# Kernel optimization log

Hardware: AMD Instinct MI355X
Metric: run time of the kernel (lower is better)

## Reference

```python
import jax, jax.numpy as jnp
import numpy as np

MASK_NEG = 1e30


def setup_inputs() -> dict:
    key = jax.random.key(0)
    k_q, k_k, k_m, k_w1, k_w2, k_v = jax.random.split(key, 6)
    B, S, D, A = 32, 2048, 1024, 1024  # batch, seq, feature dim, attn dim
    # Xavier-uniform-like scale for weights
    lim = float(np.sqrt(6.0 / (D + A)))
    query = jax.random.normal(k_q, (B, D), dtype=jnp.float32)
    keys = jax.random.normal(k_k, (B, S, D), dtype=jnp.float32)
    mask = jax.random.randint(k_m, (B, S), 0, 2) > 0  # True = keep
    W1 = jax.random.uniform(k_w1, (A, D), jnp.float32, -lim, lim)
    W2 = jax.random.uniform(k_w2, (A, D), jnp.float32, -lim, lim)
    v = jax.random.uniform(k_v, (A,), jnp.float32, -lim, lim)
    return {"query": query, "keys": keys, "mask": mask, "W1": W1, "W2": W2, "v": v}


def reference(query, keys, mask, W1, W2, v):
    w1_query = jnp.einsum('bd,ad->ba', query, W1)          # (B, A)
    w2_keys = jnp.einsum('bsd,ad->bsa', keys, W2)          # (B, S, A)
    combined = jnp.tanh(w1_query[:, None, :] + w2_keys)    # (B, S, A)
    scores = jnp.einsum('bsa,a->bs', combined, v)          # (B, S)
    # masked softmax: subtract huge constant at masked-out positions
    scores = scores - (~mask).astype(scores.dtype) * MASK_NEG
    return jax.nn.softmax(scores, axis=-1)
```

## Files before the change

kernel.cpp:

```cpp
#include <hip/hip_runtime.h>
#include <hip/hip_bf16.h>
#include <stdint.h>

#define NB 32
#define NS 2048
#define ND 1024
#define NA 1024
#define MASK_NEG 1e30f

#define BM 256
#define BN 256
#define BK 64
#define NTILES 64

typedef __attribute__((ext_vector_type(4))) float f32x4;
typedef __attribute__((ext_vector_type(8))) __bf16 bf16x8;

__device__ __forceinline__ void glds16(const void* g, void* l) {
  __builtin_amdgcn_global_load_lds(
      (const __attribute__((address_space(1))) uint32_t*)g,
      (__attribute__((address_space(3))) uint32_t*)(uintptr_t)l, 16, 0, 0);
}

__global__ __launch_bounds__(256) void cvt_bf16(const float* __restrict__ in,
                                                __bf16* __restrict__ out, int n8) {
  long i = blockIdx.x * 256 + threadIdx.x;
  const long stride = (long)gridDim.x * 256;
  for (; i < n8; i += stride) {
    f32x4 a = ((const f32x4*)in)[2 * i];
    f32x4 b = ((const f32x4*)in)[2 * i + 1];
    bf16x8 o;
#pragma unroll
    for (int j = 0; j < 4; ++j) { o[j] = (__bf16)a[j]; o[4 + j] = (__bf16)b[j]; }
    ((bf16x8*)out)[i] = o;
  }
}

__global__ __launch_bounds__(256) void w1q_kernel(const float* __restrict__ q,
                                                  const float* __restrict__ W1,
                                                  float* __restrict__ w1q) {
  const int b = blockIdx.x;
  const int a0 = blockIdx.y * 64;
  const int t = threadIdx.x;
  const int al = t >> 2;
  const int part = t & 3;
  const float* wrow = W1 + (size_t)(a0 + al) * ND + part * 256;
  const float* qrow = q + (size_t)b * ND + part * 256;
  float sum = 0.f;
#pragma unroll 8
  for (int i = 0; i < 256; i += 4) {
    float4 w = *reinterpret_cast<const float4*>(wrow + i);
    float4 x = *reinterpret_cast<const float4*>(qrow + i);
    sum += w.x * x.x + w.y * x.y + w.z * x.z + w.w * x.w;
  }
  __shared__ float red[256];
  red[t] = sum;
  __syncthreads();
  if (t < 64) {
    w1q[(size_t)b * NA + a0 + t] = red[t * 4] + red[t * 4 + 1] + red[t * 4 + 2] + red[t * 4 + 3];
  }
}

__global__ __launch_bounds__(512, 1) void score_gemm8(
    const __bf16* __restrict__ keysb, const __bf16* __restrict__ W2b,
    const float* __restrict__ w1q, const float* __restrict__ vvec,
    float* __restrict__ scores) {
  __shared__ __bf16 ldsA[4][128 * BK];
  __shared__ __bf16 ldsB[4][128 * BK];
  __shared__ float sm_w1q[NA];
  __shared__ float sm_v[NA];
  __shared__ float sm_part[4][BM];

  const int t = threadIdx.x;
  const int bs0 = blockIdx.x * BM;
  const int b = bs0 >> 11;
  const int lane = t & 63;
  const int wid = t >> 6;
  const int wr = wid >> 2;
  const int wc = wid & 3;
  const int lrow = lane & 15;
  const int ko = lane >> 4;

  for (int i = t; i < NA; i += 512) {
    sm_w1q[i] = w1q[(size_t)b * NA + i];
    sm_v[i] = vvec[i];
  }
  for (int i = t; i < 4 * BM; i += 512) ((float*)sm_part)[i] = 0.f;

  const int srow = lane >> 3;
  const int scol = (lane & 7) ^ srow;
  const size_t aoffT = (size_t)(bs0 + wid * 16 + srow) * ND + scol * 8;
  const size_t boffT = (size_t)(wid * 16 + srow) * ND + scol * 8;

  const int sl0 = ko ^ (lrow & 7);
  const int sl1 = (4 + ko) ^ (lrow & 7);

#define STAGE_A(T, H)                                                           \
  do {                                                                          \
    if ((T) < NTILES) {                                                         \
      char* d_ = (char*)ldsA + (((((T)&1) << 1) + (H)) << 14) + wid * 2048;     \
      const size_t g_ = aoffT + (size_t)((H)*128) * ND + (size_t)(((T)&15) * BK); \
      glds16(keysb + g_, d_);                                                   \
      glds16(keysb + g_ + (size_t)8 * ND, d_ + 1024);                           \
    }                                                                           \
  } while (0)

#define STAGE_B(T, H)                                                           \
  do {                                                                          \
    if ((T) < NTILES) {                                                         \
      char* d_ = (char*)ldsB + (((((T)&1) << 1) + (H)) << 14) + wid * 2048;     \
      const size_t g_ = boffT + (size_t)(((T) >> 4) * 256 + (H)*128) * ND +     \
                        (size_t)(((T)&15) * BK);                                \
      glds16(W2b + g_, d_);                                                     \
      glds16(W2b + g_ + (size_t)8 * ND, d_ + 1024);                             \
    }                                                                           \
  } while (0)

#define SB __builtin_amdgcn_sched_barrier(0)
#define P1 __builtin_amdgcn_s_setprio(1)
#define P0 __builtin_amdgcn_s_setprio(0)
#define BAR __builtin_amdgcn_s_barrier()

#define PHASE(TL, M_, N_, STAGE_STMT, WM)                                       \
  do {                                                                          \
    if ((N_) == 0) {                                                            \
      const char* Ab_ = (const char*)ldsA + (((((TL)&1) << 1) | wr) << 14);     \
      _Pragma("unroll") for (int mi = 0; mi < 4; ++mi) {                        \
        const int ra_ = (((M_)*4 + mi) * 16 + lrow) * 128;                      \
        af[mi][0] = *reinterpret_cast<const bf16x8*>(Ab_ + ra_ + sl0 * 16);     \
        af[mi][1] = *reinterpret_cast<const bf16x8*>(Ab_ + ra_ + sl1 * 16);     \
      }                                                                         \
    }                                                                           \
    {                                                                           \
      const char* Bb_ = (const char*)ldsB + (((((TL)&1) << 1) | (wc >> 1)) << 14); \
      _Pragma("unroll") for (int nq = 0; nq < 2; ++nq) {                        \
        const int rb_ = (((wc & 1) * 4 + (N_)*2 + nq) * 16 + lrow) * 128;       \
        bfr[nq][0] = *reinterpret_cast<const bf16x8*>(Bb_ + rb_ + sl0 * 16);    \
        bfr[nq][1] = *reinterpret_cast<const bf16x8*>(Bb_ + rb_ + sl1 * 16);    \
      }                                                                         \
    }                                                                           \
    STAGE_STMT;                                                                 \
    BAR;                                                                        \
    asm volatile("s_waitcnt lgkmcnt(0)");                                       \
    SB;                                                                         \
    P1;                                                                         \
    _Pragma("unroll") for (int mi = 0; mi < 4; ++mi)                            \
        _Pragma("unroll") for (int nq = 0; nq < 2; ++nq) {                      \
      acc[(M_)*4 + mi][(N_)*2 + nq] = __builtin_amdgcn_mfma_f32_16x16x32_bf16(  \
          af[mi][0], bfr[nq][0], acc[(M_)*4 + mi][(N_)*2 + nq], 0, 0, 0);       \
      acc[(M_)*4 + mi][(N_)*2 + nq] = __builtin_amdgcn_mfma_f32_16x16x32_bf16(  \
          af[mi][1], bfr[nq][1], acc[(M_)*4 + mi][(N_)*2 + nq], 0, 0, 0);       \
    }                                                                           \
    P0;                                                                         \
    if (WM) {                                                                   \
      if (it != 31) { asm volatile("s_waitcnt vmcnt(2)"); }                     \
      else { asm volatile("s_waitcnt vmcnt(0)"); }                              \
      SB;                                                                       \
    }                                                                           \
    BAR;                                                                        \
  } while (0)

  f32x4 acc[8][4];
#pragma unroll
  for (int mi = 0; mi < 8; ++mi)
#pragma unroll
    for (int ni = 0; ni < 4; ++ni) acc[mi][ni] = f32x4{0.f, 0.f, 0.f, 0.f};

  bf16x8 af[4][2], bfr[2][2];

  STAGE_A(0, 0);
  STAGE_A(0, 1);
  STAGE_B(0, 0);
  STAGE_B(0, 1);
  STAGE_A(1, 0);
  __syncthreads();

  for (int it = 0; it < 32; ++it) {
    const int t0 = 2 * it, t1 = 2 * it + 1;
    PHASE(t0, 0, 0, STAGE_A(t1, 1), 0);
    PHASE(t0, 0, 1, STAGE_B(t1, 0), 0);
    PHASE(t0, 1, 0, STAGE_B(t1, 1), 0);
    PHASE(t0, 1, 1, STAGE_A(t0 + 2, 0), 1);
    PHASE(t1, 0, 0, STAGE_A(t0 + 2, 1), 0);
    PHASE(t1, 0, 1, STAGE_B(t0 + 2, 0), 0);
    PHASE(t1, 1, 0, STAGE_B(t0 + 2, 1), 0);
    PHASE(t1, 1, 1, STAGE_A(t1 + 2, 0), 1);

    if ((it & 7) == 7) {
      const int a0 = (it >> 3) * BN;
      float w1v[4], vv[4];
#pragma unroll
      for (int ni = 0; ni < 4; ++ni) {
        const int a = a0 + wc * 64 + ni * 16 + lrow;
        w1v[ni] = sm_w1q[a];
        vv[ni] = sm_v[a];
      }
#pragma unroll
      for (int mi = 0; mi < 8; ++mi)
#pragma unroll
        for (int r = 0; r < 4; ++r) {
          float p = 0.f;
#pragma unroll
          for (int ni = 0; ni < 4; ++ni) {
            const float x = acc[mi][ni][r] + w1v[ni];
            const float e = __expf(2.f * x);
            p += (1.f - 2.f * __builtin_amdgcn_rcpf(e + 1.f)) * vv[ni];
          }
          p += __shfl_xor(p, 1);
          p += __shfl_xor(p, 2);
          p += __shfl_xor(p, 4);
          p += __shfl_xor(p, 8);
          if (lrow == 0) sm_part[wc][wr * 128 + mi * 16 + ko * 4 + r] += p;
        }
#pragma unroll
      for (int mi = 0; mi < 8; ++mi)
#pragma unroll
        for (int ni = 0; ni < 4; ++ni) acc[mi][ni] = f32x4{0.f, 0.f, 0.f, 0.f};
    }
  }

  __syncthreads();
  if (t < BM)
    scores[bs0 + t] = sm_part[0][t] + sm_part[1][t] + sm_part[2][t] + sm_part[3][t];

#undef STAGE_A
#undef STAGE_B
#undef PHASE
#undef SB
#undef P1
#undef P0
#undef BAR
}

__global__ __launch_bounds__(256) void softmax_kernel(const float* __restrict__ scores,
                                                      const int* __restrict__ mask,
                                                      float* __restrict__ out) {
  const int b = blockIdx.x;
  const int t = threadIdx.x;
  float sc[8];
  float mx = -3.4e38f;
#pragma unroll
  for (int j = 0; j < 8; ++j) {
    int i = t + j * 256;
    float s = scores[b * NS + i];
    if (mask[b * NS + i] == 0) s -= MASK_NEG;
    sc[j] = s;
    mx = fmaxf(mx, s);
  }
#pragma unroll
  for (int off = 1; off < 64; off <<= 1) mx = fmaxf(mx, __shfl_xor(mx, off));
  __shared__ float redm[4];
  __shared__ float reds[4];
  if ((t & 63) == 0) redm[t >> 6] = mx;
  __syncthreads();
  mx = fmaxf(fmaxf(redm[0], redm[1]), fmaxf(redm[2], redm[3]));
  float e[8];
  float sum = 0.f;
#pragma unroll
  for (int j = 0; j < 8; ++j) {
    e[j] = __expf(sc[j] - mx);
    sum += e[j];
  }
#pragma unroll
  for (int off = 1; off < 64; off <<= 1) sum += __shfl_xor(sum, off);
  if ((t & 63) == 0) reds[t >> 6] = sum;
  __syncthreads();
  sum = reds[0] + reds[1] + reds[2] + reds[3];
  float inv = 1.f / sum;
#pragma unroll
  for (int j = 0; j < 8; ++j) out[b * NS + t + j * 256] = e[j] * inv;
}

extern "C" void kernel_launch(void* const* d_in, const int* in_sizes, int n_in,
                              void* d_out, int out_size, void* d_ws, size_t ws_size,
                              hipStream_t stream) {
  const float* q = (const float*)d_in[0];
  const float* keysf = (const float*)d_in[1];
  const int* mask = (const int*)d_in[2];
  const float* W1 = (const float*)d_in[3];
  const float* W2f = (const float*)d_in[4];
  const float* v = (const float*)d_in[5];
  float* out = (float*)d_out;

  float* scores = (float*)d_ws;
  float* w1q = scores + NB * NS;
  __bf16* W2b = (__bf16*)(w1q + NB * NA);
  __bf16* keysb = (__bf16*)((char*)W2b + (size_t)NA * ND * 2);

  cvt_bf16<<<512, 256, 0, stream>>>(W2f, W2b, NA * ND / 8);
  cvt_bf16<<<2048, 256, 0, stream>>>(keysf, keysb, (int)((size_t)NB * NS * ND / 8));
  w1q_kernel<<<dim3(NB, NA / 64), 256, 0, stream>>>(q, W1, w1q);
  score_gemm8<<<NB * NS / BM, 512, 0, stream>>>(keysb, W2b, w1q, v, scores);
  softmax_kernel<<<NB, 256, 0, stream>>>(scores, mask, out);
}
```

Measured before the change: 253.2 us.

## Fuse fp32-to-bf16 keys conversion into score GEMM loads

```diff
diff --git a/kernel.cpp b/kernel.cpp
--- a/kernel.cpp
+++ b/kernel.cpp
@@ -20,6 +20,11 @@
   __builtin_amdgcn_global_load_lds(
       (const __attribute__((address_space(1))) uint32_t*)g,
       (__attribute__((address_space(3))) uint32_t*)(uintptr_t)l, 16, 0, 0);
+}
+
+__global__ void zero_f32(float* __restrict__ p, int n) {
+  int i = blockIdx.x * 256 + threadIdx.x;
+  if (i < n) p[i] = 0.f;
 }
 
 __global__ __launch_bounds__(256) void cvt_bf16(const float* __restrict__ in,
@@ -61,15 +66,12 @@
   }
 }
 
-__global__ __launch_bounds__(512, 1) void score_gemm8(
-    const __bf16* __restrict__ keysb, const __bf16* __restrict__ W2b,
+__global__ __launch_bounds__(512, 1) void score_gemm(
+    const float* __restrict__ keysf, const __bf16* __restrict__ W2b,
     const float* __restrict__ w1q, const float* __restrict__ vvec,
     float* __restrict__ scores) {
-  __shared__ __bf16 ldsA[4][128 * BK];
-  __shared__ __bf16 ldsB[4][128 * BK];
-  __shared__ float sm_w1q[NA];
-  __shared__ float sm_v[NA];
-  __shared__ float sm_part[4][BM];
+  __shared__ __attribute__((aligned(1024))) char ldsA[6 * 16384];
+  __shared__ __attribute__((aligned(1024))) char ldsB[4 * 16384];
 
   const int t = threadIdx.x;
   const int bs0 = blockIdx.x * BM;
@@ -81,68 +83,81 @@
   const int lrow = lane & 15;
   const int ko = lane >> 4;
 
-  for (int i = t; i < NA; i += 512) {
-    sm_w1q[i] = w1q[(size_t)b * NA + i];
-    sm_v[i] = vvec[i];
-  }
-  for (int i = t; i < 4 * BM; i += 512) ((float*)sm_part)[i] = 0.f;
-
-  const int srow = lane >> 3;
-  const int scol = (lane & 7) ^ srow;
-  const size_t aoffT = (size_t)(bs0 + wid * 16 + srow) * ND + scol * 8;
-  const size_t boffT = (size_t)(wid * 16 + srow) * ND + scol * 8;
-
-  const int sl0 = ko ^ (lrow & 7);
-  const int sl1 = (4 + ko) ^ (lrow & 7);
-
-#define STAGE_A(T, H)                                                           \
+  const int rowA = t >> 4;
+  const int scolA = (t & 15) ^ (rowA & 15);
+  const int rowB = t >> 3;
+  const int scolB = (t & 7) ^ (rowB & 7);
+
+  const int uA0 = ko * 2, uA1 = 8 + ko * 2;
+  const int sA00 = uA0 ^ lrow, sA01 = (uA0 + 1) ^ lrow;
+  const int sA10 = uA1 ^ lrow, sA11 = (uA1 + 1) ^ lrow;
+  const int sB0 = ko ^ (lrow & 7), sB1 = (4 + ko) ^ (lrow & 7);
+
+  f32x4 acc[8][4];
+#pragma unroll
+  for (int mi = 0; mi < 8; ++mi)
+#pragma unroll
+    for (int ni = 0; ni < 4; ++ni) acc[mi][ni] = f32x4{0.f, 0.f, 0.f, 0.f};
+
+  bf16x8 af[4][2], bfr[2][2];
+
+#define STAGE_A(T, Q)                                                           \
   do {                                                                          \
     if ((T) < NTILES) {                                                         \
-      char* d_ = (char*)ldsA + (((((T)&1) << 1) + (H)) << 14) + wid * 2048;     \
-      const size_t g_ = aoffT + (size_t)((H)*128) * ND + (size_t)(((T)&15) * BK); \
-      glds16(keysb + g_, d_);                                                   \
-      glds16(keysb + g_ + (size_t)8 * ND, d_ + 1024);                           \
+      const unsigned slot_ = (4u * (unsigned)(T) + (unsigned)(Q)) % 6u;         \
+      char* d_ = ldsA + slot_ * 16384 + t * 16;                                 \
+      const size_t r0_ = (size_t)(bs0 + (Q)*64 + rowA);                         \
+      const int kf_ = ((T)&15) * 64 + scolA * 4;                                \
+      glds16(keysf + r0_ * ND + kf_, d_);                                       \
+      glds16(keysf + (r0_ + 32) * ND + kf_, d_ + 8192);                         \
     }                                                                           \
   } while (0)
 
 #define STAGE_B(T, H)                                                           \
   do {                                                                          \
     if ((T) < NTILES) {                                                         \
-      char* d_ = (char*)ldsB + (((((T)&1) << 1) + (H)) << 14) + wid * 2048;     \
-      const size_t g_ = boffT + (size_t)(((T) >> 4) * 256 + (H)*128) * ND +     \
-                        (size_t)(((T)&15) * BK);                                \
-      glds16(W2b + g_, d_);                                                     \
-      glds16(W2b + g_ + (size_t)8 * ND, d_ + 1024);                             \
+      const unsigned slot_ = (2u * (unsigned)(T) + (unsigned)(H)) % 4u;         \
+      char* d_ = ldsB + slot_ * 16384 + t * 16;                                 \
+      const size_t r0_ = (size_t)(((T) >> 4) * 256 + (H)*128 + rowB);           \
+      const int ke_ = (((T)&15) * 64) + scolB * 8;                              \
+      glds16(W2b + r0_ * ND + ke_, d_);                                         \
+      glds16(W2b + (r0_ + 64) * ND + ke_, d_ + 8192);                           \
     }                                                                           \
   } while (0)
 
-#define SB __builtin_amdgcn_sched_barrier(0)
+#define SB_ __builtin_amdgcn_sched_barrier(0)
 #define P1 __builtin_amdgcn_s_setprio(1)
 #define P0 __builtin_amdgcn_s_setprio(0)
 #define BAR __builtin_amdgcn_s_barrier()
 
-#define PHASE(TL, M_, N_, STAGE_STMT, WM)                                       \
+#define PHASE(M_, N_, STAGES, WM)                                               \
   do {                                                                          \
+    STAGES;                                                                     \
     if ((N_) == 0) {                                                            \
-      const char* Ab_ = (const char*)ldsA + (((((TL)&1) << 1) | wr) << 14);     \
+      const char* Ab_ = ldsA + ((4u * (unsigned)tau + 2u * wr + (M_)) % 6u) * 16384; \
       _Pragma("unroll") for (int mi = 0; mi < 4; ++mi) {                        \
-        const int ra_ = (((M_)*4 + mi) * 16 + lrow) * 128;                      \
-        af[mi][0] = *reinterpret_cast<const bf16x8*>(Ab_ + ra_ + sl0 * 16);     \
-        af[mi][1] = *reinterpret_cast<const bf16x8*>(Ab_ + ra_ + sl1 * 16);     \
+        const int rb_ = (mi * 16 + lrow) * 256;                                 \
+        f32x4 l0 = *reinterpret_cast<const f32x4*>(Ab_ + rb_ + sA00 * 16);      \
+        f32x4 l1 = *reinterpret_cast<const f32x4*>(Ab_ + rb_ + sA01 * 16);      \
+        f32x4 h0 = *reinterpret_cast<const f32x4*>(Ab_ + rb_ + sA10 * 16);      \
+        f32x4 h1 = *reinterpret_cast<const f32x4*>(Ab_ + rb_ + sA11 * 16);      \
+        _Pragma("unroll") for (int j = 0; j < 4; ++j) {                         \
+          af[mi][0][j] = (__bf16)l0[j]; af[mi][0][4 + j] = (__bf16)l1[j];       \
+          af[mi][1][j] = (__bf16)h0[j]; af[mi][1][4 + j] = (__bf16)h1[j];       \
+        }                                                                       \
       }                                                                         \
     }                                                                           \
     {                                                                           \
-      const char* Bb_ = (const char*)ldsB + (((((TL)&1) << 1) | (wc >> 1)) << 14); \
+      const char* Bb_ = ldsB + ((2u * (unsigned)tau + (wc >> 1)) % 4u) * 16384; \
       _Pragma("unroll") for (int nq = 0; nq < 2; ++nq) {                        \
         const int rb_ = (((wc & 1) * 4 + (N_)*2 + nq) * 16 + lrow) * 128;       \
-        bfr[nq][0] = *reinterpret_cast<const bf16x8*>(Bb_ + rb_ + sl0 * 16);    \
-        bfr[nq][1] = *reinterpret_cast<const bf16x8*>(Bb_ + rb_ + sl1 * 16);    \
+        bfr[nq][0] = *reinterpret_cast<const bf16x8*>(Bb_ + rb_ + sB0 * 16);    \
+        bfr[nq][1] = *reinterpret_cast<const bf16x8*>(Bb_ + rb_ + sB1 * 16);    \
       }                                                                         \
     }                                                                           \
-    STAGE_STMT;                                                                 \
     BAR;                                                                        \
     asm volatile("s_waitcnt lgkmcnt(0)");                                       \
-    SB;                                                                         \
+    SB_;                                                                        \
     P1;                                                                         \
     _Pragma("unroll") for (int mi = 0; mi < 4; ++mi)                            \
         _Pragma("unroll") for (int nq = 0; nq < 2; ++nq) {                      \
@@ -152,48 +167,38 @@
           af[mi][1], bfr[nq][1], acc[(M_)*4 + mi][(N_)*2 + nq], 0, 0, 0);       \
     }                                                                           \
     P0;                                                                         \
-    if (WM) {                                                                   \
-      if (it != 31) { asm volatile("s_waitcnt vmcnt(2)"); }                     \
+    if ((WM) == 1) {                                                            \
+      if (tau < NTILES - 1) { asm volatile("s_waitcnt vmcnt(8)"); }             \
       else { asm volatile("s_waitcnt vmcnt(0)"); }                              \
-      SB;                                                                       \
+      SB_;                                                                      \
+    } else if ((WM) == 2) {                                                     \
+      if (tau < NTILES - 1) { asm volatile("s_waitcnt vmcnt(4)"); SB_; }        \
     }                                                                           \
     BAR;                                                                        \
   } while (0)
 
-  f32x4 acc[8][4];
-#pragma unroll
-  for (int mi = 0; mi < 8; ++mi)
-#pragma unroll
-    for (int ni = 0; ni < 4; ++ni) acc[mi][ni] = f32x4{0.f, 0.f, 0.f, 0.f};
-
-  bf16x8 af[4][2], bfr[2][2];
-
   STAGE_A(0, 0);
   STAGE_A(0, 1);
+  STAGE_A(0, 2);
+  STAGE_A(0, 3);
   STAGE_B(0, 0);
   STAGE_B(0, 1);
-  STAGE_A(1, 0);
-  __syncthreads();
-
-  for (int it = 0; it < 32; ++it) {
-    const int t0 = 2 * it, t1 = 2 * it + 1;
-    PHASE(t0, 0, 0, STAGE_A(t1, 1), 0);
-    PHASE(t0, 0, 1, STAGE_B(t1, 0), 0);
-    PHASE(t0, 1, 0, STAGE_B(t1, 1), 0);
-    PHASE(t0, 1, 1, STAGE_A(t0 + 2, 0), 1);
-    PHASE(t1, 0, 0, STAGE_A(t0 + 2, 1), 0);
-    PHASE(t1, 0, 1, STAGE_B(t0 + 2, 0), 0);
-    PHASE(t1, 1, 0, STAGE_B(t0 + 2, 1), 0);
-    PHASE(t1, 1, 1, STAGE_A(t1 + 2, 0), 1);
-
-    if ((it & 7) == 7) {
-      const int a0 = (it >> 3) * BN;
+  __syncthreads();
+
+  for (int tau = 0; tau < NTILES; ++tau) {
+    PHASE(0, 0, { STAGE_A(tau + 1, 0); STAGE_B(tau + 1, 0); }, 0);
+    PHASE(0, 1, { STAGE_A(tau + 1, 2); STAGE_B(tau + 1, 1); }, 1);
+    PHASE(1, 0, { STAGE_A(tau + 1, 1); }, 0);
+    PHASE(1, 1, { STAGE_A(tau + 1, 3); }, 2);
+
+    if ((tau & 15) == 15) {
+      const int a0 = (tau >> 4) * BN;
       float w1v[4], vv[4];
 #pragma unroll
       for (int ni = 0; ni < 4; ++ni) {
         const int a = a0 + wc * 64 + ni * 16 + lrow;
-        w1v[ni] = sm_w1q[a];
-        vv[ni] = sm_v[a];
+        w1v[ni] = w1q[(size_t)b * NA + a];
+        vv[ni] = vvec[a];
       }
 #pragma unroll
       for (int mi = 0; mi < 8; ++mi)
@@ -210,7 +215,8 @@
           p += __shfl_xor(p, 2);
           p += __shfl_xor(p, 4);
           p += __shfl_xor(p, 8);
-          if (lrow == 0) sm_part[wc][wr * 128 + mi * 16 + ko * 4 + r] += p;
+          if (lrow == 0)
+            atomicAdd(&scores[bs0 + wr * 128 + mi * 16 + ko * 4 + r], p);
         }
 #pragma unroll
       for (int mi = 0; mi < 8; ++mi)
@@ -218,15 +224,11 @@
         for (int ni = 0; ni < 4; ++ni) acc[mi][ni] = f32x4{0.f, 0.f, 0.f, 0.f};
     }
   }
-
-  __syncthreads();
-  if (t < BM)
-    scores[bs0 + t] = sm_part[0][t] + sm_part[1][t] + sm_part[2][t] + sm_part[3][t];
 
 #undef STAGE_A
 #undef STAGE_B
 #undef PHASE
-#undef SB
+#undef SB_
 #undef P1
 #undef P0
 #undef BAR
@@ -285,11 +287,10 @@
   float* scores = (float*)d_ws;
   float* w1q = scores + NB * NS;
   __bf16* W2b = (__bf16*)(w1q + NB * NA);
-  __bf16* keysb = (__bf16*)((char*)W2b + (size_t)NA * ND * 2);
-
+
+  zero_f32<<<NB * NS / 256, 256, 0, stream>>>(scores, NB * NS);
   cvt_bf16<<<512, 256, 0, stream>>>(W2f, W2b, NA * ND / 8);
-  cvt_bf16<<<2048, 256, 0, stream>>>(keysf, keysb, (int)((size_t)NB * NS * ND / 8));
   w1q_kernel<<<dim3(NB, NA / 64), 256, 0, stream>>>(q, W1, w1q);
-  score_gemm8<<<NB * NS / BM, 512, 0, stream>>>(keysb, W2b, w1q, v, scores);
+  score_gemm<<<NB * NS / BM, 512, 0, stream>>>(keysf, W2b, w1q, v, scores);
   softmax_kernel<<<NB, 256, 0, stream>>>(scores, mask, out);
 }
```

Result: faster. 236.3 us (-6.7%).

## Deepen A-operand LDS ring to three stages and issue loads before fragment reads

Applied to the files above, without the earlier changes.

```diff
diff --git a/kernel.cpp b/kernel.cpp
--- a/kernel.cpp
+++ b/kernel.cpp
@@ -20,6 +20,11 @@
   __builtin_amdgcn_global_load_lds(
       (const __attribute__((address_space(1))) uint32_t*)g,
       (__attribute__((address_space(3))) uint32_t*)(uintptr_t)l, 16, 0, 0);
+}
+
+__global__ void zero_f32(float* __restrict__ p, int n) {
+  int i = blockIdx.x * 256 + threadIdx.x;
+  if (i < n) p[i] = 0.f;
 }
 
 __global__ __launch_bounds__(256) void cvt_bf16(const float* __restrict__ in,
@@ -65,11 +70,8 @@
     const __bf16* __restrict__ keysb, const __bf16* __restrict__ W2b,
     const float* __restrict__ w1q, const float* __restrict__ vvec,
     float* __restrict__ scores) {
-  __shared__ __bf16 ldsA[4][128 * BK];
+  __shared__ __bf16 ldsA[6][128 * BK];
   __shared__ __bf16 ldsB[4][128 * BK];
-  __shared__ float sm_w1q[NA];
-  __shared__ float sm_v[NA];
-  __shared__ float sm_part[4][BM];
 
   const int t = threadIdx.x;
   const int bs0 = blockIdx.x * BM;
@@ -81,12 +83,6 @@
   const int lrow = lane & 15;
   const int ko = lane >> 4;
 
-  for (int i = t; i < NA; i += 512) {
-    sm_w1q[i] = w1q[(size_t)b * NA + i];
-    sm_v[i] = vvec[i];
-  }
-  for (int i = t; i < 4 * BM; i += 512) ((float*)sm_part)[i] = 0.f;
-
   const int srow = lane >> 3;
   const int scol = (lane & 7) ^ srow;
   const size_t aoffT = (size_t)(bs0 + wid * 16 + srow) * ND + scol * 8;
@@ -98,7 +94,8 @@
 #define STAGE_A(T, H)                                                           \
   do {                                                                          \
     if ((T) < NTILES) {                                                         \
-      char* d_ = (char*)ldsA + (((((T)&1) << 1) + (H)) << 14) + wid * 2048;     \
+      const unsigned slot_ = (2u * (unsigned)(T) + (unsigned)(H)) % 6u;         \
+      char* d_ = (char*)ldsA + (slot_ << 14) + wid * 2048;                      \
       const size_t g_ = aoffT + (size_t)((H)*128) * ND + (size_t)(((T)&15) * BK); \
       glds16(keysb + g_, d_);                                                   \
       glds16(keysb + g_ + (size_t)8 * ND, d_ + 1024);                           \
@@ -108,7 +105,8 @@
 #define STAGE_B(T, H)                                                           \
   do {                                                                          \
     if ((T) < NTILES) {                                                         \
-      char* d_ = (char*)ldsB + (((((T)&1) << 1) + (H)) << 14) + wid * 2048;     \
+      const unsigned slot_ = (2u * (unsigned)(T) + (unsigned)(H)) % 4u;         \
+      char* d_ = (char*)ldsB + (slot_ << 14) + wid * 2048;                      \
       const size_t g_ = boffT + (size_t)(((T) >> 4) * 256 + (H)*128) * ND +     \
                         (size_t)(((T)&15) * BK);                                \
       glds16(W2b + g_, d_);                                                     \
@@ -123,8 +121,10 @@
 
 #define PHASE(TL, M_, N_, STAGE_STMT, WM)                                       \
   do {                                                                          \
+    STAGE_STMT;                                                                 \
     if ((N_) == 0) {                                                            \
-      const char* Ab_ = (const char*)ldsA + (((((TL)&1) << 1) | wr) << 14);     \
+      const char* Ab_ =                                                         \
+          (const char*)ldsA + (((2u * (unsigned)(TL) + (unsigned)wr) % 6u) << 14); \
       _Pragma("unroll") for (int mi = 0; mi < 4; ++mi) {                        \
         const int ra_ = (((M_)*4 + mi) * 16 + lrow) * 128;                      \
         af[mi][0] = *reinterpret_cast<const bf16x8*>(Ab_ + ra_ + sl0 * 16);     \
@@ -132,14 +132,14 @@
       }                                                                         \
     }                                                                           \
     {                                                                           \
-      const char* Bb_ = (const char*)ldsB + (((((TL)&1) << 1) | (wc >> 1)) << 14); \
+      const char* Bb_ =                                                         \
+          (const char*)ldsB + (((2u * (unsigned)(TL) + (unsigned)(wc >> 1)) % 4u) << 14); \
       _Pragma("unroll") for (int nq = 0; nq < 2; ++nq) {                        \
         const int rb_ = (((wc & 1) * 4 + (N_)*2 + nq) * 16 + lrow) * 128;       \
         bfr[nq][0] = *reinterpret_cast<const bf16x8*>(Bb_ + rb_ + sl0 * 16);    \
         bfr[nq][1] = *reinterpret_cast<const bf16x8*>(Bb_ + rb_ + sl1 * 16);    \
       }                                                                         \
     }                                                                           \
-    STAGE_STMT;                                                                 \
     BAR;                                                                        \
     asm volatile("s_waitcnt lgkmcnt(0)");                                       \
     SB;                                                                         \
@@ -153,7 +153,7 @@
     }                                                                           \
     P0;                                                                         \
     if (WM) {                                                                   \
-      if (it != 31) { asm volatile("s_waitcnt vmcnt(2)"); }                     \
+      if (it != 31) { asm volatile("s_waitcnt vmcnt(4)"); }                     \
       else { asm volatile("s_waitcnt vmcnt(0)"); }                              \
       SB;                                                                       \
     }                                                                           \
@@ -170,21 +170,22 @@
 
   STAGE_A(0, 0);
   STAGE_A(0, 1);
+  STAGE_A(1, 0);
+  STAGE_A(1, 1);
   STAGE_B(0, 0);
   STAGE_B(0, 1);
-  STAGE_A(1, 0);
   __syncthreads();
 
   for (int it = 0; it < 32; ++it) {
     const int t0 = 2 * it, t1 = 2 * it + 1;
-    PHASE(t0, 0, 0, STAGE_A(t1, 1), 0);
-    PHASE(t0, 0, 1, STAGE_B(t1, 0), 0);
-    PHASE(t0, 1, 0, STAGE_B(t1, 1), 0);
-    PHASE(t0, 1, 1, STAGE_A(t0 + 2, 0), 1);
-    PHASE(t1, 0, 0, STAGE_A(t0 + 2, 1), 0);
-    PHASE(t1, 0, 1, STAGE_B(t0 + 2, 0), 0);
-    PHASE(t1, 1, 0, STAGE_B(t0 + 2, 1), 0);
-    PHASE(t1, 1, 1, STAGE_A(t1 + 2, 0), 1);
+    PHASE(t0, 0, 0, STAGE_B(t1, 0), 0);
+    PHASE(t0, 0, 1, STAGE_B(t1, 1), 0);
+    PHASE(t0, 1, 0, STAGE_A(t0 + 2, 0), 0);
+    PHASE(t0, 1, 1, STAGE_A(t0 + 2, 1), 1);
+    PHASE(t1, 0, 0, STAGE_B(t0 + 2, 0), 0);
+    PHASE(t1, 0, 1, { STAGE_B(t0 + 2, 1); STAGE_A(t1 + 2, 0); }, 0);
+    PHASE(t1, 1, 0, STAGE_A(t1 + 2, 1), 0);
+    PHASE(t1, 1, 1, {}, 1);
 
     if ((it & 7) == 7) {
       const int a0 = (it >> 3) * BN;
@@ -192,8 +193,8 @@
 #pragma unroll
       for (int ni = 0; ni < 4; ++ni) {
         const int a = a0 + wc * 64 + ni * 16 + lrow;
-        w1v[ni] = sm_w1q[a];
-        vv[ni] = sm_v[a];
+        w1v[ni] = w1q[(size_t)b * NA + a];
+        vv[ni] = vvec[a];
       }
 #pragma unroll
       for (int mi = 0; mi < 8; ++mi)
@@ -210,7 +211,8 @@
           p += __shfl_xor(p, 2);
           p += __shfl_xor(p, 4);
           p += __shfl_xor(p, 8);
-          if (lrow == 0) sm_part[wc][wr * 128 + mi * 16 + ko * 4 + r] += p;
+          if (lrow == 0)
+            atomicAdd(&scores[bs0 + wr * 128 + mi * 16 + ko * 4 + r], p);
         }
 #pragma unroll
       for (int mi = 0; mi < 8; ++mi)
@@ -218,10 +220,6 @@
         for (int ni = 0; ni < 4; ++ni) acc[mi][ni] = f32x4{0.f, 0.f, 0.f, 0.f};
     }
   }
-
-  __syncthreads();
-  if (t < BM)
-    scores[bs0 + t] = sm_part[0][t] + sm_part[1][t] + sm_part[2][t] + sm_part[3][t];
 
 #undef STAGE_A
 #undef STAGE_B
@@ -287,6 +285,7 @@
   __bf16* W2b = (__bf16*)(w1q + NB * NA);
   __bf16* keysb = (__bf16*)((char*)W2b + (size_t)NA * ND * 2);
 
+  zero_f32<<<NB * NS / 256, 256, 0, stream>>>(scores, NB * NS);
   cvt_bf16<<<512, 256, 0, stream>>>(W2f, W2b, NA * ND / 8);
   cvt_bf16<<<2048, 256, 0, stream>>>(keysf, keysb, (int)((size_t)NB * NS * ND / 8));
   w1q_kernel<<<dim3(NB, NA / 64), 256, 0, stream>>>(q, W1, w1q);
```

Measured after the change: 257.5 us. Within noise of the previous version (+1.7%).
